# Optimization experiments

Measured on AMD Instinct MI355X. Metric: run time of the kernel, lower is better.

## Reference

```python
import jax, jax.numpy as jnp
import numpy as np

SHAPES = ((100, 152), (50, 76), (25, 38), (13, 19))  # per-level (H, W), stride 8/16/32/64 of 800x1216
S_TOTAL = sum(h * w for h, w in SHAPES)  # 20197
D, H, LVL, P, NL, H2 = 256, 8, 4, 4, 6, 2
B, NQ_TOTAL, NPROP = 8, 350, 300
DFF = 1024


def layer_norm(x, w, b, eps=1e-5):
    m = jnp.mean(x, -1, keepdims=True)
    v = jnp.mean((x - m) ** 2, -1, keepdims=True)
    return (x - m) / jnp.sqrt(v + eps) * w + b


def pos2posemb(pos, num_pos_feats=64, temperature=10000.0):
    pos = pos * (2.0 * np.pi)
    dim_t = temperature ** (2.0 * (jnp.arange(num_pos_feats) // 2).astype(jnp.float32) / num_pos_feats)
    pe = pos[..., None] / dim_t  # [..., 4, 64]
    pe = jnp.stack((jnp.sin(pe[..., 0::2]), jnp.cos(pe[..., 1::2])), axis=-1)  # [..., 4, 32, 2]
    return pe.reshape(pe.shape[:-3] + (-1,))  # [..., 256]


def bilinear_gather(v_l, loc, hl, wl):
    # v_l [B, hl*wl, H, Dh]; loc [B, Nq, H, P, 2] in [0,1]; grid_sample align_corners=False, zero padding
    b, nq, h, p, _ = loc.shape
    dh = v_l.shape[-1]
    x = loc[..., 0] * wl - 0.5
    y = loc[..., 1] * hl - 0.5
    x0 = jnp.floor(x)
    y0 = jnp.floor(y)
    lx = x - x0
    ly = y - y0

    def g(xi, yi):
        valid = (xi >= 0) & (xi <= wl - 1) & (yi >= 0) & (yi <= hl - 1)
        xi_i = jnp.clip(xi, 0, wl - 1).astype(jnp.int32)
        yi_i = jnp.clip(yi, 0, hl - 1).astype(jnp.int32)
        idx = (yi_i * wl + xi_i).transpose(0, 1, 3, 2).reshape(b, nq * p, h)  # per-head spatial index
        out = jnp.take_along_axis(v_l, jnp.broadcast_to(idx[..., None], (b, nq * p, h, dh)), axis=1)
        out = out.reshape(b, nq, p, h, dh).transpose(0, 1, 3, 2, 4)  # [B,Nq,H,P,Dh]
        return out * valid.astype(v_l.dtype)[..., None]

    return (g(x0, y0) * ((1 - lx) * (1 - ly))[..., None]
            + g(x0 + 1, y0) * (lx * (1 - ly))[..., None]
            + g(x0, y0 + 1) * ((1 - lx) * ly)[..., None]
            + g(x0 + 1, y0 + 1) * (lx * ly)[..., None])


def ms_deform_attn(query, ref, src, Woff, boff, Wa, ba, Wv, bv, Wout, bout):
    b, nq, d = query.shape
    dh = d // H
    value = (src @ Wv + bv).reshape(b, -1, H, dh)
    off = (query @ Woff + boff).reshape(b, nq, H, LVL, P, 2)
    attn = jax.nn.softmax((query @ Wa + ba).reshape(b, nq, H, LVL * P), -1).reshape(b, nq, H, LVL, P)
    # 4-d reference points: center + offsets scaled by box size
    loc = ref[:, :, None, :, None, :2] + off / P * ref[:, :, None, :, None, 2:] * 0.5  # [b,nq,H,L,P,2]
    out = jnp.zeros((b, nq, H, dh), query.dtype)
    start = 0
    for l, (hl, wl) in enumerate(SHAPES):
        v_l = value[:, start:start + hl * wl]
        start += hl * wl
        samp = bilinear_gather(v_l, loc[:, :, :, l], hl, wl)  # [b,nq,H,P,dh]
        out = out + (samp * attn[:, :, :, l, :, None]).sum(3)
    return out.reshape(b, nq, d) @ Wout + bout


def weight_attn(q_in, k_in, Wq, bq, Wk, bk):
    b, nq, d = q_in.shape
    nk = k_in.shape[1]
    dh = d // H2
    q = (q_in @ Wq + bq).reshape(b, nq, H2, dh).transpose(0, 2, 1, 3)
    k = (k_in @ Wk + bk).reshape(b, nk, H2, dh).transpose(0, 2, 1, 3)
    mm = jax.nn.softmax(jnp.einsum('bhqd,bhkd->bhqk', q, k) * (1.0 / dh ** 0.5), -1)
    qn = q / (jnp.linalg.norm(q, axis=-1, keepdims=True) + 1e-6)
    kn = k / (jnp.linalg.norm(k, axis=-1, keepdims=True) + 1e-6)
    cos = jnp.einsum('bhqd,bhkd->bhqk', qn, kn)
    return cos, mm


def setup_inputs():
    key = jax.random.key(0)
    ks = jax.random.split(key, 32)
    f = jnp.float32
    inp = {}
    inp['tgt'] = jax.random.normal(ks[0], (B, NQ_TOTAL, D), f)
    inp['reference_points'] = jax.random.uniform(ks[1], (B, NQ_TOTAL, 4), f, 0.05, 0.95)
    inp['src'] = jax.random.normal(ks[2], (B, S_TOTAL, D), f)
    inp['src_spatial_shapes'] = jnp.array(SHAPES, jnp.int32)
    lsi = np.cumsum([0] + [h * w for h, w in SHAPES])[:-1]
    inp['src_level_start_index'] = jnp.array(lsi, jnp.int32)
    inp['src_valid_ratios'] = jnp.ones((B, LVL, 2), f)
    inp['num_proposals'] = NPROP
    names = [('Woff', (NL, D, H * LVL * P * 2)), ('boff', (NL, H * LVL * P * 2)),
             ('Wa', (NL, D, H * LVL * P)), ('ba', (NL, H * LVL * P)),
             ('Wv', (NL, D, D)), ('bv', (NL, D)), ('Wout', (NL, D, D)), ('bout', (NL, D)),
             ('Wl1', (NL, D, DFF)), ('bl1', (NL, DFF)), ('Wl2', (NL, DFF, D)), ('bl2', (NL, D)),
             ('Wq', (NL, D, D)), ('bq', (NL, D)), ('Wk', (NL, D, D)), ('bk', (NL, D))]
    for i, (n, s) in enumerate(names):
        inp[n] = jax.random.normal(ks[3 + i], s, f) * 0.02
    inp['n1w'] = jnp.ones((NL, D), f)
    inp['n1b'] = jnp.zeros((NL, D), f)
    inp['n3w'] = jnp.ones((NL, D), f)
    inp['n3b'] = jnp.zeros((NL, D), f)
    return inp


def reference(tgt, reference_points, src, src_spatial_shapes, src_level_start_index,
              src_valid_ratios, num_proposals, Woff, boff, Wa, ba, Wv, bv, Wout, bout,
              Wl1, bl1, Wl2, bl2, Wq, bq, Wk, bk, n1w, n1b, n3w, n3b):
    proposals = tgt[:, :num_proposals]
    track_queries = tgt[:, num_proposals:]
    p_ref = reference_points[:, :num_proposals]
    t_ref = reference_points[:, num_proposals:]
    vr = jnp.concatenate([src_valid_ratios, src_valid_ratios], -1)  # [B,L,4]
    ref_input = p_ref[:, :, None] * vr[:, None]  # [B,Np,L,4]
    p_pos = pos2posemb(p_ref)
    t_pos = pos2posemb(t_ref)  # computed per torch code; WeightAttention ignores pos
    for l in range(NL):
        q = proposals + p_pos
        ca = ms_deform_attn(q, ref_input, src, Woff[l], boff[l], Wa[l], ba[l], Wv[l], bv[l], Wout[l], bout[l])
        proposals = layer_norm(proposals + ca, n1w[l], n1b[l])  # dropout = identity (eval)
        ffn = jax.nn.relu(proposals @ Wl1[l] + bl1[l]) @ Wl2[l] + bl2[l]
        proposals = layer_norm(proposals + ffn, n3w[l], n3b[l])
        pt_cos, pt_mm = weight_attn(proposals, track_queries, Wq[l], bq[l], Wk[l], bk[l])
        pp_cos, pp_mm = weight_attn(proposals, proposals, Wq[l], bq[l], Wk[l], bk[l])
    return proposals, p_ref, pt_cos, pp_cos, pt_mm, pp_mm
```

## Files before the change

### kernel.cpp

```cpp
#include <hip/hip_runtime.h>

#define BB 8
#define NQ 300
#define NTQ 50
#define NLAY 6
#define S_TOTAL 20197
#define ROWS (BB*NQ)
#define MVAL (BB*S_TOTAL)

typedef unsigned short u16;
typedef unsigned int u32;
typedef __bf16 v8bf __attribute__((ext_vector_type(8)));
typedef float f32x4 __attribute__((ext_vector_type(4)));

__device__ __forceinline__ u16 f2b(float f) {
    u32 u = __float_as_uint(f);
    u32 r = (u + 0x7fffu + ((u >> 16) & 1u)) >> 16;
    return (u16)r;
}
__device__ __forceinline__ u32 pk2(float lo, float hi) {
    return (u32)f2b(lo) | ((u32)f2b(hi) << 16);
}

#define ASYNC_CP16(dst_lds, src_g) \
    __builtin_amdgcn_global_load_lds((const __attribute__((address_space(1))) u32*)(src_g), \
                                     (__attribute__((address_space(3))) u32*)(dst_lds), 16, 0, 0)

__global__ void transpose_pack(
    const float* Woff, const float* Wa, const float* Wv, const float* Wout,
    const float* Wl1, const float* Wl2, const float* Wq, const float* Wk,
    const float* boff, const float* ba, const float* bvp, const float* bout,
    const float* bl1, const float* bl2, const float* bq, const float* bk,
    u16* wt, float* bias)
{
    int idx = blockIdx.x * 256 + threadIdx.x;
    if (idx < 5308416) {
        int l = idx / 884736;
        int o = idx % 884736;
        float v;
        if (o < 98304) { int n = o >> 8, k = o & 255;
            v = (n < 256) ? Woff[l*65536 + k*256 + n] : Wa[l*32768 + k*128 + (n-256)];
        } else if (o < 163840) { int o2 = o - 98304; int n = o2 >> 8, k = o2 & 255;
            v = Wv[l*65536 + k*256 + n];
        } else if (o < 229376) { int o2 = o - 163840; int n = o2 >> 8, k = o2 & 255;
            v = Wout[l*65536 + k*256 + n];
        } else if (o < 491520) { int o2 = o - 229376; int n = o2 >> 8, k = o2 & 255;
            v = Wl1[l*262144 + k*1024 + n];
        } else if (o < 753664) { int o2 = o - 491520; int n = o2 >> 10, k = o2 & 1023;
            v = Wl2[l*262144 + k*256 + n];
        } else { int o2 = o - 753664; int n = o2 >> 8, k = o2 & 255;
            v = (n < 256) ? Wq[l*65536 + k*256 + n] : Wk[l*65536 + k*256 + (n-256)];
        }
        wt[idx] = f2b(v);
    } else {
        int i2 = idx - 5308416;
        if (i2 < 16128) {
            int l = i2 / 2688, o = i2 % 2688;
            float v;
            if (o < 256)       v = boff[l*256 + o];
            else if (o < 384)  v = ba  [l*128 + (o-256)];
            else if (o < 640)  v = bvp [l*256 + (o-384)];
            else if (o < 896)  v = bout[l*256 + (o-640)];
            else if (o < 1920) v = bl1 [l*1024 + (o-896)];
            else if (o < 2176) v = bl2 [l*256 + (o-1920)];
            else if (o < 2432) v = bq  [l*256 + (o-2176)];
            else               v = bk  [l*256 + (o-2432)];
            bias[i2] = v;
        }
    }
}

__global__ void src_convert(const float* __restrict__ src, u16* __restrict__ dst)
{
    long i = ((long)blockIdx.x*256 + threadIdx.x)*8;
    float4 a = *(const float4*)(src+i), b4 = *(const float4*)(src+i+4);
    uint4 o = make_uint4(pk2(a.x,a.y), pk2(a.z,a.w), pk2(b4.x,b4.y), pk2(b4.z,b4.w));
    *(uint4*)&dst[i] = o;
}

__global__ void setup_kernel(const float* tgt, const float* refp, float* prop,
                             u16* q_b, float* ppos, u16* tq, float* out_pref)
{
    int row = blockIdx.x, t = threadIdx.x;
    if (row < ROWS) {
        int b = row / NQ, q = row % NQ;
        int k = t >> 6, rem = t & 63, j = rem >> 1;
        float pr = refp[(b*350 + q)*4 + k];
        float dimt = powf(10000.0f, (float)j * (1.0f/32.0f));
        float arg = pr * 6.283185307179586f / dimt;
        float pe = (rem & 1) ? cosf(arg) : sinf(arg);
        ppos[row*256 + t] = pe;
        float pv = tgt[(b*350 + q)*256 + t];
        prop[row*256 + t] = pv;
        q_b[row*256 + t] = f2b(pv + pe);
        if (t < 4) out_pref[row*4 + t] = refp[(b*350 + q)*4 + t];
    } else {
        int r2 = row - ROWS;
        int b = r2 / NTQ, qq = r2 % NTQ;
        tq[r2*256 + t] = f2b(tgt[(b*350 + NQ + qq)*256 + t]);
    }
}

__global__ __launch_bounds__(256) void gemm_bt(
    const u16* __restrict__ A, const u16* __restrict__ Bt,
    const float* __restrict__ bias, void* __restrict__ Cout,
    int M, int N, int K, int flags)
{
    __shared__ __align__(16) u16 As[128*32];
    __shared__ __align__(16) u16 Bs[128*32];
    int tid = threadIdx.x;
    int lane = tid & 63, wave = tid >> 6;
    int bm = blockIdx.y * 128, bn = blockIdx.x * 128;
    int wm = (wave >> 1) * 64, wn = (wave & 1) * 64;
    f32x4 acc[4][4] = {};
    int r = tid >> 2, c = (tid & 3) * 8;
    const u16* Ap0 = A  + (long)min(bm + r,      M-1) * K + c;
    const u16* Ap1 = A  + (long)min(bm + r + 64, M-1) * K + c;
    const u16* Bp0 = Bt + (long)min(bn + r,      N-1) * K + c;
    const u16* Bp1 = Bt + (long)min(bn + r + 64, N-1) * K + c;
    u16* lA0 = &As[tid*8];
    u16* lA1 = &As[64*32 + tid*8];
    u16* lB0 = &Bs[tid*8];
    u16* lB1 = &Bs[64*32 + tid*8];
    int fr = lane & 15, fk = (lane >> 4) * 8;

    for (int k0 = 0; k0 < K; k0 += 32) {
        ASYNC_CP16(lA0, Ap0 + k0);
        ASYNC_CP16(lA1, Ap1 + k0);
        ASYNC_CP16(lB0, Bp0 + k0);
        ASYNC_CP16(lB1, Bp1 + k0);
        __syncthreads();
        v8bf af[4], bf[4];
        #pragma unroll
        for (int i = 0; i < 4; ++i) af[i] = *(const v8bf*)&As[(wm + i*16 + fr)*32 + fk];
        #pragma unroll
        for (int j = 0; j < 4; ++j) bf[j] = *(const v8bf*)&Bs[(wn + j*16 + fr)*32 + fk];
        #pragma unroll
        for (int i = 0; i < 4; ++i)
            #pragma unroll
            for (int j = 0; j < 4; ++j)
                acc[i][j] = __builtin_amdgcn_mfma_f32_16x16x32_bf16(af[i], bf[j], acc[i][j], 0, 0, 0);
        __syncthreads();
    }
    int cq = lane >> 4, cn = lane & 15;
    #pragma unroll
    for (int i = 0; i < 4; ++i) {
        #pragma unroll
        for (int j = 0; j < 4; ++j) {
            int col = bn + wn + j*16 + cn;
            float bv_ = bias ? bias[col] : 0.0f;
            #pragma unroll
            for (int rr = 0; rr < 4; ++rr) {
                int m = bm + wm + i*16 + cq*4 + rr;
                if (m < M) {
                    float v = acc[i][j][rr] + bv_;
                    if (flags & 1) v = fmaxf(v, 0.0f);
                    if (flags & 2) ((u16*)Cout)[(long)m*N + col] = f2b(v);
                    else           ((float*)Cout)[(long)m*N + col] = v;
                }
            }
        }
    }
}

__global__ __launch_bounds__(256) void gemm_value6(
    const u16* __restrict__ A, const u16* __restrict__ wtall,
    const float* __restrict__ biasall, u16* __restrict__ Cout)
{
    __shared__ __align__(16) u16 As[128*32];
    __shared__ __align__(16) u16 Bs[128*32];
    const int nwg = 12*1263;
    int bid = blockIdx.x;
    int q_ = nwg >> 3, r_ = nwg & 7;
    int xcd = bid & 7, sl = bid >> 3;
    int wgid = (xcd < r_ ? xcd*(q_+1) : r_*(q_+1) + (xcd - r_)*q_) + sl;
    int y = wgid / 12, zx = wgid - y*12;
    int z = zx >> 1;
    int bm = y*128, bn = (zx & 1)*128;
    const u16* Bt = wtall + (size_t)z*884736 + 98304;
    const float* bs = biasall + z*2688 + 384;
    u16* Cz = Cout + (size_t)z*((size_t)MVAL*256);

    int tid = threadIdx.x;
    int lane = tid & 63, wave = tid >> 6;
    int wm = (wave >> 1) * 64, wn = (wave & 1) * 64;
    f32x4 acc[4][4] = {};
    int r = tid >> 2, c = (tid & 3) * 8;
    const u16* Ap0 = A  + (long)min(bm + r,      MVAL-1) * 256 + c;
    const u16* Ap1 = A  + (long)min(bm + r + 64, MVAL-1) * 256 + c;
    const u16* Bp0 = Bt + (long)(bn + r)      * 256 + c;
    const u16* Bp1 = Bt + (long)(bn + r + 64) * 256 + c;
    u16* lA0 = &As[tid*8];
    u16* lA1 = &As[64*32 + tid*8];
    u16* lB0 = &Bs[tid*8];
    u16* lB1 = &Bs[64*32 + tid*8];
    int fr = lane & 15, fk = (lane >> 4) * 8;

    for (int k0 = 0; k0 < 256; k0 += 32) {
        ASYNC_CP16(lA0, Ap0 + k0);
        ASYNC_CP16(lA1, Ap1 + k0);
        ASYNC_CP16(lB0, Bp0 + k0);
        ASYNC_CP16(lB1, Bp1 + k0);
        __syncthreads();
        v8bf af[4], bf[4];
        #pragma unroll
        for (int i = 0; i < 4; ++i) af[i] = *(const v8bf*)&As[(wm + i*16 + fr)*32 + fk];
        #pragma unroll
        for (int j = 0; j < 4; ++j) bf[j] = *(const v8bf*)&Bs[(wn + j*16 + fr)*32 + fk];
        #pragma unroll
        for (int i = 0; i < 4; ++i)
            #pragma unroll
            for (int j = 0; j < 4; ++j)
                acc[i][j] = __builtin_amdgcn_mfma_f32_16x16x32_bf16(af[i], bf[j], acc[i][j], 0, 0, 0);
        __syncthreads();
    }
    int cq = lane >> 4, cn = lane & 15;
    #pragma unroll
    for (int i = 0; i < 4; ++i) {
        #pragma unroll
        for (int j = 0; j < 4; ++j) {
            int col = bn + wn + j*16 + cn;
            float bv_ = bs[col];
            #pragma unroll
            for (int rr = 0; rr < 4; ++rr) {
                int m = bm + wm + i*16 + cq*4 + rr;
                if (m < MVAL)
                    Cz[(long)m*256 + col] = f2b(acc[i][j][rr] + bv_);
            }
        }
    }
}

__global__ __launch_bounds__(256) void sample_fused(
    const u16* __restrict__ value, const float* __restrict__ offatt,
    const float* __restrict__ refp, const float* __restrict__ svr,
    u16* __restrict__ sampout)
{
    int row = blockIdx.x, t = threadIdx.x;
    int b = row / NQ, q = row % NQ;
    __shared__ float lg[128], awl[128], sxl[128], syl[128];
    const int WL[4] = {152,76,38,19}, HL[4] = {100,50,25,13}, LS[4] = {0,15200,19000,19950};

    if (t < 128) lg[t] = offatt[row*384 + 256 + t];
    __syncthreads();
    if (t < 128) {
        int h = t >> 4, s = t & 15, lvl = s >> 2, pp = s & 3;
        int gb = h << 4;
        float mx = -1e30f;
        for (int i = 0; i < 16; ++i) mx = fmaxf(mx, lg[gb + i]);
        float sm = 0.f;
        for (int i = 0; i < 16; ++i) sm += expf(lg[gb + i] - mx);
        awl[t] = expf(lg[t] - mx) / sm;
        float rx = refp[(b*350+q)*4 + 0] * svr[(b*4+lvl)*2 + 0];
        float ry = refp[(b*350+q)*4 + 1] * svr[(b*4+lvl)*2 + 1];
        float rw = refp[(b*350+q)*4 + 2] * svr[(b*4+lvl)*2 + 0];
        float rh = refp[(b*350+q)*4 + 3] * svr[(b*4+lvl)*2 + 1];
        float ox = offatt[row*384 + h*32 + lvl*8 + pp*2 + 0];
        float oy = offatt[row*384 + h*32 + lvl*8 + pp*2 + 1];
        sxl[t] = (rx + ox * 0.25f * rw * 0.5f) * (float)WL[lvl] - 0.5f;
        syl[t] = (ry + oy * 0.25f * rh * 0.5f) * (float)HL[lvl] - 0.5f;
    }
    __syncthreads();

    int lane = t & 63, wv = t >> 6;
    int g = lane >> 3, e = lane & 7;
    for (int hh = 0; hh < 2; ++hh) {
        int h = wv*2 + hh;
        float a0 = 0.f, a1 = 0.f, a2 = 0.f, a3 = 0.f;
        #pragma unroll
        for (int it = 0; it < 8; ++it) {
            int task = it*8 + g;
            int s = task >> 2, cc = task & 3;
            int cx = cc & 1, cy = cc >> 1;
            int lvl = s >> 2;
            float x = sxl[h*16 + s], y2 = syl[h*16 + s], aw = awl[h*16 + s];
            float x0 = floorf(x), y0 = floorf(y2);
            float xc = x0 + (float)cx, yc = y0 + (float)cy;
            int wl = WL[lvl], hl = HL[lvl];
            if (xc >= 0.f && xc <= (float)(wl-1) && yc >= 0.f && yc <= (float)(hl-1)) {
                float lx = x - x0, ly = y2 - y0;
                float wgt = aw * (cx ? lx : 1.f - lx) * (cy ? ly : 1.f - ly);
                long off = ((long)b*S_TOTAL + LS[lvl] + (int)yc*wl + (int)xc)*256 + h*32 + e*4;
                uint2 v = *(const uint2*)(value + off);
                a0 += wgt * __uint_as_float((v.x & 0xffffu) << 16);
                a1 += wgt * __uint_as_float(v.x & 0xffff0000u);
                a2 += wgt * __uint_as_float((v.y & 0xffffu) << 16);
                a3 += wgt * __uint_as_float(v.y & 0xffff0000u);
            }
        }
        #pragma unroll
        for (int o = 8; o < 64; o <<= 1) {
            a0 += __shfl_xor(a0, o); a1 += __shfl_xor(a1, o);
            a2 += __shfl_xor(a2, o); a3 += __shfl_xor(a3, o);
        }
        if (g == 0)
            *(uint2*)&sampout[row*256 + h*32 + e*4] = make_uint2(pk2(a0, a1), pk2(a2, a3));
    }
}

__global__ void ln_kernel(float* __restrict__ prop, const float* __restrict__ delta,
                          const float* __restrict__ w, const float* __restrict__ bsh,
                          u16* __restrict__ pb_out, u16* __restrict__ q_out,
                          const float* __restrict__ ppos)
{
    int row = blockIdx.x, t = threadIdx.x;
    int lane = t & 63, wv = t >> 6;
    float v = prop[row*256 + t] + delta[row*256 + t];
    float s = v;
    for (int o = 32; o; o >>= 1) s += __shfl_xor(s, o);
    __shared__ float red[4], red2[4];
    if (lane == 0) red[wv] = s;
    __syncthreads();
    float mean = (red[0]+red[1]+red[2]+red[3]) * (1.0f/256.0f);
    float dd = v - mean;
    float s2 = dd * dd;
    for (int o = 32; o; o >>= 1) s2 += __shfl_xor(s2, o);
    if (lane == 0) red2[wv] = s2;
    __syncthreads();
    float var = (red2[0]+red2[1]+red2[2]+red2[3]) * (1.0f/256.0f);
    float nv = dd * rsqrtf(var + 1e-5f) * w[t] + bsh[t];
    prop[row*256 + t] = nv;
    pb_out[row*256 + t] = f2b(nv);
    if (q_out) q_out[row*256 + t] = f2b(nv + ppos[row*256 + t]);
}

__global__ __launch_bounds__(128) void qk_convert(
    const float* __restrict__ qkp, const float* __restrict__ kt,
    u16* __restrict__ qk_b, u16* __restrict__ kt_b,
    float* __restrict__ qn_g, float* __restrict__ knp_g, float* __restrict__ knt_g)
{
    int row = blockIdx.x, t = threadIdx.x;
    __shared__ float part[128];
    if (row < ROWS) {
        const float* sp = qkp + (long)row*512 + t*4;
        float4 v = *(const float4*)sp;
        *(uint2*)&qk_b[(long)row*512 + t*4] = make_uint2(pk2(v.x,v.y), pk2(v.z,v.w));
        part[t] = v.x*v.x + v.y*v.y + v.z*v.z + v.w*v.w;
        __syncthreads();
        if (t < 4) {
            float s = 0.f;
            for (int i = 0; i < 32; ++i) s += part[t*32 + i];
            int b = row / NQ, q = row % NQ;
            float nv = sqrtf(s) + 1e-6f;
            if      (t == 0) qn_g [(b*2+0)*NQ + q] = nv;
            else if (t == 1) qn_g [(b*2+1)*NQ + q] = nv;
            else if (t == 2) knp_g[(b*2+0)*NQ + q] = nv;
            else             knp_g[(b*2+1)*NQ + q] = nv;
        }
    } else {
        int r2 = row - ROWS;
        float ss = 0.f;
        if (t < 64) {
            const float* sp = kt + (long)r2*256 + t*4;
            float4 v = *(const float4*)sp;
            *(uint2*)&kt_b[(long)r2*256 + t*4] = make_uint2(pk2(v.x,v.y), pk2(v.z,v.w));
            ss = v.x*v.x + v.y*v.y + v.z*v.z + v.w*v.w;
        }
        part[t] = ss;
        __syncthreads();
        if (t < 2) {
            float s = 0.f;
            for (int i = 0; i < 32; ++i) s += part[t*32 + i];
            int b = r2 / NTQ, qq = r2 % NTQ;
            knt_g[(b*2+t)*NTQ + qq] = sqrtf(s) + 1e-6f;
        }
    }
}

__global__ __launch_bounds__(256) void wattn_mfma(
    const u16* __restrict__ Qb, const u16* __restrict__ Kb,
    int qstride, int kstride, int koff, int nk,
    const float* __restrict__ qn_g, const float* __restrict__ kn_g,
    float* __restrict__ out_cos, float* __restrict__ out_logit)
{
    __shared__ __align__(16) u16 As[128*32];
    __shared__ __align__(16) u16 Bs[128*32];
    int bh = blockIdx.z, b = bh >> 1, h = bh & 1;
    int tid = threadIdx.x;
    int lane = tid & 63, wave = tid >> 6;
    int bm = blockIdx.y * 128, bn = blockIdx.x * 128;
    int wm = (wave >> 1) * 64, wn = (wave & 1) * 64;
    f32x4 acc[4][4] = {};
    int r = tid >> 2, c = (tid & 3) * 8;
    const u16* Ap0 = Qb + (long)(b*NQ + min(bm + r,      NQ-1))*qstride + h*128 + c;
    const u16* Ap1 = Qb + (long)(b*NQ + min(bm + r + 64, NQ-1))*qstride + h*128 + c;
    const u16* Bp0 = Kb + (long)(b*nk + min(bn + r,      nk-1))*kstride + koff + h*128 + c;
    const u16* Bp1 = Kb + (long)(b*nk + min(bn + r + 64, nk-1))*kstride + koff + h*128 + c;
    u16* lA0 = &As[tid*8];
    u16* lA1 = &As[64*32 + tid*8];
    u16* lB0 = &Bs[tid*8];
    u16* lB1 = &Bs[64*32 + tid*8];
    int fr = lane & 15, fk = (lane >> 4) * 8;

    for (int k0 = 0; k0 < 128; k0 += 32) {
        ASYNC_CP16(lA0, Ap0 + k0);
        ASYNC_CP16(lA1, Ap1 + k0);
        ASYNC_CP16(lB0, Bp0 + k0);
        ASYNC_CP16(lB1, Bp1 + k0);
        __syncthreads();
        v8bf af[4], bf[4];
        #pragma unroll
        for (int i = 0; i < 4; ++i) af[i] = *(const v8bf*)&As[(wm + i*16 + fr)*32 + fk];
        #pragma unroll
        for (int j = 0; j < 4; ++j) bf[j] = *(const v8bf*)&Bs[(wn + j*16 + fr)*32 + fk];
        #pragma unroll
        for (int i = 0; i < 4; ++i)
            #pragma unroll
            for (int j = 0; j < 4; ++j)
                acc[i][j] = __builtin_amdgcn_mfma_f32_16x16x32_bf16(af[i], bf[j], acc[i][j], 0, 0, 0);
        __syncthreads();
    }
    const float SC = 0.08838834764831845f;
    int cq = lane >> 4, cn = lane & 15;
    #pragma unroll
    for (int i = 0; i < 4; ++i) {
        #pragma unroll
        for (int j = 0; j < 4; ++j) {
            int col = bn + wn + j*16 + cn;
            #pragma unroll
            for (int rr = 0; rr < 4; ++rr) {
                int m = bm + wm + i*16 + cq*4 + rr;
                if (m < NQ && col < nk) {
                    float d = acc[i][j][rr];
                    long o = ((long)(bh*NQ + m))*nk + col;
                    out_cos[o]   = d / (qn_g[bh*NQ + m] * kn_g[bh*nk + col]);
                    out_logit[o] = d * SC;
                }
            }
        }
    }
}

__global__ __launch_bounds__(64) void row_softmax(float* __restrict__ buf, int nk)
{
    long row = blockIdx.x;
    float* p = buf + row*nk;
    int lane = threadIdx.x;
    float mx = -1e30f;
    for (int k = lane; k < nk; k += 64) mx = fmaxf(mx, p[k]);
    for (int o = 32; o; o >>= 1) mx = fmaxf(mx, __shfl_xor(mx, o));
    float s = 0.f;
    for (int k = lane; k < nk; k += 64) s += expf(p[k] - mx);
    for (int o = 32; o; o >>= 1) s += __shfl_xor(s, o);
    float inv = 1.0f / s;
    for (int k = lane; k < nk; k += 64) p[k] = expf(p[k] - mx) * inv;
}

__global__ void writeout_kernel(const float* __restrict__ prop, float* __restrict__ out)
{
    int row = blockIdx.x, t = threadIdx.x;
    out[row*256 + t] = prop[row*256 + t];
}

extern "C" void kernel_launch(void* const* d_in, const int* in_sizes, int n_in,
                              void* d_out, int out_size, void* d_ws, size_t ws_size,
                              hipStream_t stream)
{
    (void)in_sizes; (void)n_in; (void)out_size; (void)ws_size;
    const float* tgt  = (const float*)d_in[0];
    const float* refp = (const float*)d_in[1];
    const float* src  = (const float*)d_in[2];
    const float* svr  = (const float*)d_in[5];
    const float* Woff = (const float*)d_in[7];
    const float* boff = (const float*)d_in[8];
    const float* Wa   = (const float*)d_in[9];
    const float* ba   = (const float*)d_in[10];
    const float* Wv   = (const float*)d_in[11];
    const float* bv   = (const float*)d_in[12];
    const float* Wout = (const float*)d_in[13];
    const float* bout = (const float*)d_in[14];
    const float* Wl1  = (const float*)d_in[15];
    const float* bl1  = (const float*)d_in[16];
    const float* Wl2  = (const float*)d_in[17];
    const float* bl2  = (const float*)d_in[18];
    const float* Wq   = (const float*)d_in[19];
    const float* bq   = (const float*)d_in[20];
    const float* Wk   = (const float*)d_in[21];
    const float* bk   = (const float*)d_in[22];
    const float* n1w  = (const float*)d_in[23];
    const float* n1b  = (const float*)d_in[24];
    const float* n3w  = (const float*)d_in[25];
    const float* n3b  = (const float*)d_in[26];
    float* out = (float*)d_out;

    char* p = (char*)d_ws;
    auto alloc = [&](size_t bytes) { void* r = (void*)p; p += (bytes + 255) & ~(size_t)255; return r; };
    u16*   wt      = (u16*)  alloc(6ull*884736*2);
    float* bias    = (float*)alloc(6ull*2688*4);
    u16*   value   = (u16*)  alloc(6ull*MVAL*256*2);
    u16*   src_b   = (u16*)  alloc((size_t)MVAL*256*2);
    float* prop    = (float*)alloc((size_t)ROWS*256*4);
    u16*   prop_b  = (u16*)  alloc((size_t)ROWS*256*2);
    u16*   q_b     = (u16*)  alloc((size_t)ROWS*256*2);
    float* ppos    = (float*)alloc((size_t)ROWS*256*4);
    float* offatt  = (float*)alloc((size_t)ROWS*384*4);
    u16*   sampout = (u16*)  alloc((size_t)ROWS*256*2);
    float* ca      = (float*)alloc((size_t)ROWS*256*4);
    u16*   ff1     = (u16*)  alloc((size_t)ROWS*1024*2);
    float* ff2     = (float*)alloc((size_t)ROWS*256*4);
    u16*   tq      = (u16*)  alloc(400ull*256*2);
    float* qkp     = (float*)alloc((size_t)ROWS*512*4);
    float* kt      = (float*)alloc(400ull*256*4);
    u16*   qk_b    = (u16*)  alloc((size_t)ROWS*512*2);
    u16*   kt_b    = (u16*)  alloc(400ull*256*2);
    float* qn_g    = (float*)alloc(16ull*NQ*4);
    float* knp_g   = (float*)alloc(16ull*NQ*4);
    float* knt_g   = (float*)alloc(16ull*NTQ*4);

    transpose_pack<<<20799, 256, 0, stream>>>(Woff, Wa, Wv, Wout, Wl1, Wl2, Wq, Wk,
                                              boff, ba, bv, bout, bl1, bl2, bq, bk, wt, bias);
    src_convert<<<20197, 256, 0, stream>>>(src, src_b);
    setup_kernel<<<ROWS + 400, 256, 0, stream>>>(tgt, refp, prop, q_b, ppos, tq, out + 614400);
    gemm_value6<<<12*1263, 256, 0, stream>>>(src_b, wt, bias, value);

    for (int l = 0; l < NLAY; ++l) {
        const u16* wl_ = wt + (size_t)l*884736;
        const float* bl_ = bias + l*2688;
        gemm_bt<<<dim3(3, 19),   256, 0, stream>>>(q_b,    wl_,          bl_,        offatt, ROWS, 384, 256, 0);
        sample_fused<<<ROWS, 256, 0, stream>>>(value + (size_t)l*MVAL*256, offatt, refp, svr, sampout);
        gemm_bt<<<dim3(2, 19),   256, 0, stream>>>(sampout, wl_ + 163840, bl_ + 640,  ca,    ROWS, 256, 256, 0);
        ln_kernel<<<ROWS, 256, 0, stream>>>(prop, ca, n1w + l*256, n1b + l*256, prop_b, (u16*)nullptr, ppos);
        gemm_bt<<<dim3(8, 19),   256, 0, stream>>>(prop_b, wl_ + 229376, bl_ + 896,  ff1,   ROWS, 1024, 256, 3);
        gemm_bt<<<dim3(2, 19),   256, 0, stream>>>(ff1,    wl_ + 491520, bl_ + 1920, ff2,   ROWS, 256, 1024, 0);
        ln_kernel<<<ROWS, 256, 0, stream>>>(prop, ff2, n3w + l*256, n3b + l*256, prop_b, q_b, ppos);
    }

    const u16* w5 = wt + 5ull*884736;
    const float* b5 = bias + 5*2688;
    gemm_bt<<<dim3(4, 19), 256, 0, stream>>>(prop_b, w5 + 753664,         b5 + 2176,       qkp, ROWS, 512, 256, 0);
    gemm_bt<<<dim3(2, 4),  256, 0, stream>>>(tq,     w5 + 753664 + 65536, b5 + 2176 + 256, kt,  400,  256, 256, 0);
    qk_convert<<<2800, 128, 0, stream>>>(qkp, kt, qk_b, kt_b, qn_g, knp_g, knt_g);
    wattn_mfma<<<dim3(1, 3, 16), 256, 0, stream>>>(qk_b, kt_b, 512, 256, 0,   NTQ, qn_g, knt_g,
                                                   out + 624000, out + 2304000);
    wattn_mfma<<<dim3(3, 3, 16), 256, 0, stream>>>(qk_b, qk_b, 512, 512, 256, NQ,  qn_g, knp_g,
                                                   out + 864000, out + 2544000);
    row_softmax<<<4800, 64, 0, stream>>>(out + 2304000, NTQ);
    row_softmax<<<4800, 64, 0, stream>>>(out + 2544000, NQ);
    writeout_kernel<<<ROWS, 256, 0, stream>>>(prop, out);
}
```

Baseline: 1.500 ms.

## Double-buffer LDS in MFMA GEMMs and add 64-row tile variant for small GEMMs

Converts every MFMA GEMM kernel (gemm_bt, gemm_value6, wattn_mfma) to double-buffered LDS, issuing the async copy for the next K-slice before computing on the current one, so global loads overlap the MFMA work. Adds a gemm_bt64 kernel with 64-row M tiles and switches the per-layer and final projection GEMMs to it. This doubles the block count for these small-M GEMMs (2400 rows), giving better CU occupancy. The cost is doubled LDS per block and an explicit vmcnt wait each iteration.

```diff
diff --git a/kernel.cpp b/kernel.cpp
--- a/kernel.cpp
+++ b/kernel.cpp
@@ -106,8 +106,8 @@
     const float* __restrict__ bias, void* __restrict__ Cout,
     int M, int N, int K, int flags)
 {
-    __shared__ __align__(16) u16 As[128*32];
-    __shared__ __align__(16) u16 Bs[128*32];
+    __shared__ __align__(16) u16 As[2][128*32];
+    __shared__ __align__(16) u16 Bs[2][128*32];
     int tid = threadIdx.x;
     int lane = tid & 63, wave = tid >> 6;
     int bm = blockIdx.y * 128, bn = blockIdx.x * 128;
@@ -118,29 +118,33 @@
     const u16* Ap1 = A  + (long)min(bm + r + 64, M-1) * K + c;
     const u16* Bp0 = Bt + (long)min(bn + r,      N-1) * K + c;
     const u16* Bp1 = Bt + (long)min(bn + r + 64, N-1) * K + c;
-    u16* lA0 = &As[tid*8];
-    u16* lA1 = &As[64*32 + tid*8];
-    u16* lB0 = &Bs[tid*8];
-    u16* lB1 = &Bs[64*32 + tid*8];
     int fr = lane & 15, fk = (lane >> 4) * 8;
 
+    auto STG = [&](int bi, int k0) {
+        ASYNC_CP16(&As[bi][tid*8],         Ap0 + k0);
+        ASYNC_CP16(&As[bi][64*32 + tid*8], Ap1 + k0);
+        ASYNC_CP16(&Bs[bi][tid*8],         Bp0 + k0);
+        ASYNC_CP16(&Bs[bi][64*32 + tid*8], Bp1 + k0);
+    };
+    STG(0, 0);
+    asm volatile("s_waitcnt vmcnt(0)" ::: "memory");
+    __syncthreads();
+    int cur = 0;
     for (int k0 = 0; k0 < K; k0 += 32) {
-        ASYNC_CP16(lA0, Ap0 + k0);
-        ASYNC_CP16(lA1, Ap1 + k0);
-        ASYNC_CP16(lB0, Bp0 + k0);
-        ASYNC_CP16(lB1, Bp1 + k0);
-        __syncthreads();
+        if (k0 + 32 < K) STG(cur ^ 1, k0 + 32);
         v8bf af[4], bf[4];
         #pragma unroll
-        for (int i = 0; i < 4; ++i) af[i] = *(const v8bf*)&As[(wm + i*16 + fr)*32 + fk];
-        #pragma unroll
-        for (int j = 0; j < 4; ++j) bf[j] = *(const v8bf*)&Bs[(wn + j*16 + fr)*32 + fk];
+        for (int i = 0; i < 4; ++i) af[i] = *(const v8bf*)&As[cur][(wm + i*16 + fr)*32 + fk];
+        #pragma unroll
+        for (int j = 0; j < 4; ++j) bf[j] = *(const v8bf*)&Bs[cur][(wn + j*16 + fr)*32 + fk];
         #pragma unroll
         for (int i = 0; i < 4; ++i)
             #pragma unroll
             for (int j = 0; j < 4; ++j)
                 acc[i][j] = __builtin_amdgcn_mfma_f32_16x16x32_bf16(af[i], bf[j], acc[i][j], 0, 0, 0);
+        asm volatile("s_waitcnt vmcnt(0)" ::: "memory");
         __syncthreads();
+        cur ^= 1;
     }
     int cq = lane >> 4, cn = lane & 15;
     #pragma unroll
@@ -163,12 +167,76 @@
     }
 }
 
+__global__ __launch_bounds__(256) void gemm_bt64(
+    const u16* __restrict__ A, const u16* __restrict__ Bt,
+    const float* __restrict__ bias, void* __restrict__ Cout,
+    int M, int N, int K, int flags)
+{
+    __shared__ __align__(16) u16 As[2][64*32];
+    __shared__ __align__(16) u16 Bs[2][128*32];
+    int tid = threadIdx.x;
+    int lane = tid & 63, wave = tid >> 6;
+    int bm = blockIdx.y * 64, bn = blockIdx.x * 128;
+    int wm = (wave >> 1) * 32, wn = (wave & 1) * 64;
+    f32x4 acc[2][4] = {};
+    int r = tid >> 2, c = (tid & 3) * 8;
+    const u16* Ap0 = A  + (long)min(bm + r,      M-1) * K + c;
+    const u16* Bp0 = Bt + (long)min(bn + r,      N-1) * K + c;
+    const u16* Bp1 = Bt + (long)min(bn + r + 64, N-1) * K + c;
+    int fr = lane & 15, fk = (lane >> 4) * 8;
+
+    auto STG = [&](int bi, int k0) {
+        ASYNC_CP16(&As[bi][tid*8],         Ap0 + k0);
+        ASYNC_CP16(&Bs[bi][tid*8],         Bp0 + k0);
+        ASYNC_CP16(&Bs[bi][64*32 + tid*8], Bp1 + k0);
+    };
+    STG(0, 0);
+    asm volatile("s_waitcnt vmcnt(0)" ::: "memory");
+    __syncthreads();
+    int cur = 0;
+    for (int k0 = 0; k0 < K; k0 += 32) {
+        if (k0 + 32 < K) STG(cur ^ 1, k0 + 32);
+        v8bf af[2], bf[4];
+        #pragma unroll
+        for (int i = 0; i < 2; ++i) af[i] = *(const v8bf*)&As[cur][(wm + i*16 + fr)*32 + fk];
+        #pragma unroll
+        for (int j = 0; j < 4; ++j) bf[j] = *(const v8bf*)&Bs[cur][(wn + j*16 + fr)*32 + fk];
+        #pragma unroll
+        for (int i = 0; i < 2; ++i)
+            #pragma unroll
+            for (int j = 0; j < 4; ++j)
+                acc[i][j] = __builtin_amdgcn_mfma_f32_16x16x32_bf16(af[i], bf[j], acc[i][j], 0, 0, 0);
+        asm volatile("s_waitcnt vmcnt(0)" ::: "memory");
+        __syncthreads();
+        cur ^= 1;
+    }
+    int cq = lane >> 4, cn = lane & 15;
+    #pragma unroll
+    for (int i = 0; i < 2; ++i) {
+        #pragma unroll
+        for (int j = 0; j < 4; ++j) {
+            int col = bn + wn + j*16 + cn;
+            float bv_ = bias ? bias[col] : 0.0f;
+            #pragma unroll
+            for (int rr = 0; rr < 4; ++rr) {
+                int m = bm + wm + i*16 + cq*4 + rr;
+                if (m < M) {
+                    float v = acc[i][j][rr] + bv_;
+                    if (flags & 1) v = fmaxf(v, 0.0f);
+                    if (flags & 2) ((u16*)Cout)[(long)m*N + col] = f2b(v);
+                    else           ((float*)Cout)[(long)m*N + col] = v;
+                }
+            }
+        }
+    }
+}
+
 __global__ __launch_bounds__(256) void gemm_value6(
     const u16* __restrict__ A, const u16* __restrict__ wtall,
     const float* __restrict__ biasall, u16* __restrict__ Cout)
 {
-    __shared__ __align__(16) u16 As[128*32];
-    __shared__ __align__(16) u16 Bs[128*32];
+    __shared__ __align__(16) u16 As[2][128*32];
+    __shared__ __align__(16) u16 Bs[2][128*32];
     const int nwg = 12*1263;
     int bid = blockIdx.x;
     int q_ = nwg >> 3, r_ = nwg & 7;
@@ -190,29 +258,33 @@
     const u16* Ap1 = A  + (long)min(bm + r + 64, MVAL-1) * 256 + c;
     const u16* Bp0 = Bt + (long)(bn + r)      * 256 + c;
     const u16* Bp1 = Bt + (long)(bn + r + 64) * 256 + c;
-    u16* lA0 = &As[tid*8];
-    u16* lA1 = &As[64*32 + tid*8];
-    u16* lB0 = &Bs[tid*8];
-    u16* lB1 = &Bs[64*32 + tid*8];
     int fr = lane & 15, fk = (lane >> 4) * 8;
 
+    auto STG = [&](int bi, int k0) {
+        ASYNC_CP16(&As[bi][tid*8],         Ap0 + k0);
+        ASYNC_CP16(&As[bi][64*32 + tid*8], Ap1 + k0);
+        ASYNC_CP16(&Bs[bi][tid*8],         Bp0 + k0);
+        ASYNC_CP16(&Bs[bi][64*32 + tid*8], Bp1 + k0);
+    };
+    STG(0, 0);
+    asm volatile("s_waitcnt vmcnt(0)" ::: "memory");
+    __syncthreads();
+    int cur = 0;
     for (int k0 = 0; k0 < 256; k0 += 32) {
-        ASYNC_CP16(lA0, Ap0 + k0);
-        ASYNC_CP16(lA1, Ap1 + k0);
-        ASYNC_CP16(lB0, Bp0 + k0);
-        ASYNC_CP16(lB1, Bp1 + k0);
-        __syncthreads();
+        if (k0 + 32 < 256) STG(cur ^ 1, k0 + 32);
         v8bf af[4], bf[4];
         #pragma unroll
-        for (int i = 0; i < 4; ++i) af[i] = *(const v8bf*)&As[(wm + i*16 + fr)*32 + fk];
-        #pragma unroll
-        for (int j = 0; j < 4; ++j) bf[j] = *(const v8bf*)&Bs[(wn + j*16 + fr)*32 + fk];
+        for (int i = 0; i < 4; ++i) af[i] = *(const v8bf*)&As[cur][(wm + i*16 + fr)*32 + fk];
+        #pragma unroll
+        for (int j = 0; j < 4; ++j) bf[j] = *(const v8bf*)&Bs[cur][(wn + j*16 + fr)*32 + fk];
         #pragma unroll
         for (int i = 0; i < 4; ++i)
             #pragma unroll
             for (int j = 0; j < 4; ++j)
                 acc[i][j] = __builtin_amdgcn_mfma_f32_16x16x32_bf16(af[i], bf[j], acc[i][j], 0, 0, 0);
+        asm volatile("s_waitcnt vmcnt(0)" ::: "memory");
         __syncthreads();
+        cur ^= 1;
     }
     int cq = lane >> 4, cn = lane & 15;
     #pragma unroll
@@ -373,8 +445,8 @@
     const float* __restrict__ qn_g, const float* __restrict__ kn_g,
     float* __restrict__ out_cos, float* __restrict__ out_logit)
 {
-    __shared__ __align__(16) u16 As[128*32];
-    __shared__ __align__(16) u16 Bs[128*32];
+    __shared__ __align__(16) u16 As[2][128*32];
+    __shared__ __align__(16) u16 Bs[2][128*32];
     int bh = blockIdx.z, b = bh >> 1, h = bh & 1;
     int tid = threadIdx.x;
     int lane = tid & 63, wave = tid >> 6;
@@ -386,29 +458,33 @@
     const u16* Ap1 = Qb + (long)(b*NQ + min(bm + r + 64, NQ-1))*qstride + h*128 + c;
     const u16* Bp0 = Kb + (long)(b*nk + min(bn + r,      nk-1))*kstride + koff + h*128 + c;
     const u16* Bp1 = Kb + (long)(b*nk + min(bn + r + 64, nk-1))*kstride + koff + h*128 + c;
-    u16* lA0 = &As[tid*8];
-    u16* lA1 = &As[64*32 + tid*8];
-    u16* lB0 = &Bs[tid*8];
-    u16* lB1 = &Bs[64*32 + tid*8];
     int fr = lane & 15, fk = (lane >> 4) * 8;
 
+    auto STG = [&](int bi, int k0) {
+        ASYNC_CP16(&As[bi][tid*8],         Ap0 + k0);
+        ASYNC_CP16(&As[bi][64*32 + tid*8], Ap1 + k0);
+        ASYNC_CP16(&Bs[bi][tid*8],         Bp0 + k0);
+        ASYNC_CP16(&Bs[bi][64*32 + tid*8], Bp1 + k0);
+    };
+    STG(0, 0);
+    asm volatile("s_waitcnt vmcnt(0)" ::: "memory");
+    __syncthreads();
+    int cur = 0;
     for (int k0 = 0; k0 < 128; k0 += 32) {
-        ASYNC_CP16(lA0, Ap0 + k0);
-        ASYNC_CP16(lA1, Ap1 + k0);
-        ASYNC_CP16(lB0, Bp0 + k0);
-        ASYNC_CP16(lB1, Bp1 + k0);
-        __syncthreads();
+        if (k0 + 32 < 128) STG(cur ^ 1, k0 + 32);
         v8bf af[4], bf[4];
         #pragma unroll
-        for (int i = 0; i < 4; ++i) af[i] = *(const v8bf*)&As[(wm + i*16 + fr)*32 + fk];
-        #pragma unroll
-        for (int j = 0; j < 4; ++j) bf[j] = *(const v8bf*)&Bs[(wn + j*16 + fr)*32 + fk];
+        for (int i = 0; i < 4; ++i) af[i] = *(const v8bf*)&As[cur][(wm + i*16 + fr)*32 + fk];
+        #pragma unroll
+        for (int j = 0; j < 4; ++j) bf[j] = *(const v8bf*)&Bs[cur][(wn + j*16 + fr)*32 + fk];
         #pragma unroll
         for (int i = 0; i < 4; ++i)
             #pragma unroll
             for (int j = 0; j < 4; ++j)
                 acc[i][j] = __builtin_amdgcn_mfma_f32_16x16x32_bf16(af[i], bf[j], acc[i][j], 0, 0, 0);
+        asm volatile("s_waitcnt vmcnt(0)" ::: "memory");
         __syncthreads();
+        cur ^= 1;
     }
     const float SC = 0.08838834764831845f;
     int cq = lane >> 4, cn = lane & 15;
@@ -516,19 +592,19 @@
     for (int l = 0; l < NLAY; ++l) {
         const u16* wl_ = wt + (size_t)l*884736;
         const float* bl_ = bias + l*2688;
-        gemm_bt<<<dim3(3, 19),   256, 0, stream>>>(q_b,    wl_,          bl_,        offatt, ROWS, 384, 256, 0);
+        gemm_bt64<<<dim3(3, 38), 256, 0, stream>>>(q_b,    wl_,          bl_,        offatt, ROWS, 384, 256, 0);
         sample_fused<<<ROWS, 256, 0, stream>>>(value + (size_t)l*MVAL*256, offatt, refp, svr, sampout);
-        gemm_bt<<<dim3(2, 19),   256, 0, stream>>>(sampout, wl_ + 163840, bl_ + 640,  ca,    ROWS, 256, 256, 0);
+        gemm_bt64<<<dim3(2, 38), 256, 0, stream>>>(sampout, wl_ + 163840, bl_ + 640,  ca,    ROWS, 256, 256, 0);
         ln_kernel<<<ROWS, 256, 0, stream>>>(prop, ca, n1w + l*256, n1b + l*256, prop_b, (u16*)nullptr, ppos);
-        gemm_bt<<<dim3(8, 19),   256, 0, stream>>>(prop_b, wl_ + 229376, bl_ + 896,  ff1,   ROWS, 1024, 256, 3);
-        gemm_bt<<<dim3(2, 19),   256, 0, stream>>>(ff1,    wl_ + 491520, bl_ + 1920, ff2,   ROWS, 256, 1024, 0);
+        gemm_bt64<<<dim3(8, 38), 256, 0, stream>>>(prop_b, wl_ + 229376, bl_ + 896,  ff1,   ROWS, 1024, 256, 3);
+        gemm_bt64<<<dim3(2, 38), 256, 0, stream>>>(ff1,    wl_ + 491520, bl_ + 1920, ff2,   ROWS, 256, 1024, 0);
         ln_kernel<<<ROWS, 256, 0, stream>>>(prop, ff2, n3w + l*256, n3b + l*256, prop_b, q_b, ppos);
     }
 
     const u16* w5 = wt + 5ull*884736;
     const float* b5 = bias + 5*2688;
-    gemm_bt<<<dim3(4, 19), 256, 0, stream>>>(prop_b, w5 + 753664,         b5 + 2176,       qkp, ROWS, 512, 256, 0);
-    gemm_bt<<<dim3(2, 4),  256, 0, stream>>>(tq,     w5 + 753664 + 65536, b5 + 2176 + 256, kt,  400,  256, 256, 0);
+    gemm_bt64<<<dim3(4, 38), 256, 0, stream>>>(prop_b, w5 + 753664,         b5 + 2176,       qkp, ROWS, 512, 256, 0);
+    gemm_bt64<<<dim3(2, 7),  256, 0, stream>>>(tq,     w5 + 753664 + 65536, b5 + 2176 + 256, kt,  400,  256, 256, 0);
     qk_convert<<<2800, 128, 0, stream>>>(qkp, kt, qk_b, kt_b, qn_g, knp_g, knt_g);
     wattn_mfma<<<dim3(1, 3, 16), 256, 0, stream>>>(qk_b, kt_b, 512, 256, 0,   NTQ, qn_g, knt_g,
                                                    out + 624000, out + 2304000);
```

Result: faster. 1.300 ms (-13.3%).
